# Performance work log

Hardware: AMD Instinct MI355X
Metric: run time of the kernel (lower is better)

The kernel has to match this reference:

```python
import jax, jax.numpy as jnp
import numpy as np

TEMPERATURE = 12.5      # args_temperature
SINKHORN_EPS = 0.05     # entropic regularization replacing exact cv2.EMD
SINKHORN_ITERS = 100


def _sinkhorn_flow(cost, a, b):
    # cost: [N, hw, hw] (rows=query nodes, cols=proto nodes)
    # a: [N, hw] row marginals, b: [N, hw] col marginals (each sums to hw)
    K = jnp.exp(-cost / SINKHORN_EPS)
    v0 = jnp.ones_like(b)

    def body(v, _):
        u = a / (jnp.einsum('nuv,nv->nu', K, v) + 1e-30)
        v = b / (jnp.einsum('nuv,nu->nv', K, u) + 1e-30)
        return v, None

    v, _ = jax.lax.scan(body, v0, None, length=SINKHORN_ITERS)
    u = a / (jnp.einsum('nuv,nv->nu', K, v) + 1e-30)
    return u[:, :, None] * K * v[:, None, :]  # transport plan [N, hw, hw]


def setup_inputs() -> dict:
    key = jax.random.key(0)
    k1, k2 = jax.random.split(key)
    shape = (8, 5, 15, 640, 5, 5)  # (b, n2, n1, c, h, w)
    return {
        'in_support': jax.random.normal(k1, shape, jnp.float32),
        'in_query': jax.random.normal(k2, shape, jnp.float32),
    }


def reference(in_support, in_query):
    b, n2, n1, c, h, w = in_support.shape
    N, hw = b * n2 * n1, h * w
    S = in_support.reshape(N, c, hw)  # support/proto nodes
    Q = in_query.reshape(N, c, hw)    # query nodes

    # get_weight_vector: relu(<node, global-avg-pool(other)>) + 0.001
    w1 = jax.nn.relu(jnp.einsum('nck,nc->nk', Q, S.mean(-1))) + 0.001  # query-side
    w2 = jax.nn.relu(jnp.einsum('nck,nc->nk', S, Q.mean(-1))) + 0.001  # proto-side

    # normalize_feature: subtract per-sample channel mean ('center')
    S = S - S.mean(axis=1, keepdims=True)
    Q = Q - Q.mean(axis=1, keepdims=True)

    # cosine similarity map: sim[u, v] = cos(query_node_u, proto_node_v)
    Sn = S / jnp.maximum(jnp.linalg.norm(S, axis=1, keepdims=True), 1e-8)
    Qn = Q / jnp.maximum(jnp.linalg.norm(Q, axis=1, keepdims=True), 1e-8)
    sim = jnp.einsum('ncu,ncv->nuv', Qn, Sn)  # [N, hw, hw]

    # emd marginals: (w + 1e-5) rescaled so each sums to hw
    a = w1 + 1e-5
    a = a * (hw / a.sum(-1, keepdims=True))
    bm = w2 + 1e-5
    bm = bm * (hw / bm.sum(-1, keepdims=True))

    # OT flow on cost = 1 - sim (flow treated as a constant, like cv2 detach)
    flow = jax.lax.stop_gradient(_sinkhorn_flow(1.0 - sim, a, bm))

    return (sim * flow).sum((-1, -2)) * (TEMPERATURE / hw)  # logits [N]
```

## Files before the change

### kernel.cpp

```cpp
#include <hip/hip_runtime.h>

typedef short bf16x8 __attribute__((ext_vector_type(8)));
typedef float f32x4  __attribute__((ext_vector_type(4)));

constexpr int C  = 640;
constexpr int HW = 25;
constexpr int CHUNK  = 128;
constexpr int NCHUNK = 5;

__device__ __forceinline__ float rl(float x, int lane) {
  return __uint_as_float(__builtin_amdgcn_readlane(__float_as_uint(x), lane));
}

__device__ __forceinline__ void split_bf16(float x, unsigned& h, unsigned& l) {
  unsigned u = __float_as_uint(x);
  unsigned hb = (u + 0x7FFFu + ((u >> 16) & 1u)) >> 16;
  float hf = __uint_as_float(hb << 16);
  float lo = x - hf;
  unsigned ul = __float_as_uint(lo);
  unsigned lb = (ul + 0x7FFFu + ((ul >> 16) & 1u)) >> 16;
  h = hb; l = lb;
}

__global__ __launch_bounds__(256) void emd_fused(
    const float* __restrict__ support, const float* __restrict__ query,
    float* __restrict__ out)
{
  const int n = blockIdx.x, tid = threadIdx.x;

  __shared__ __attribute__((aligned(16))) unsigned short planes[4 * 32 * CHUNK];
  __shared__ float G[625];
  __shared__ float scr[4][200];
  __shared__ float sQv[25], sSv[25], nqv[25], nsv[25], amv[25], bmv[25], scal[2];

  const float* Qg = query   + (size_t)n * (C * HW);
  const float* Sg = support + (size_t)n * (C * HW);

  for (int g = tid; g < 448; g += 256) {
    int pl = g / 112, rem = g % 112;
    int r = 25 + rem / 16, cq = rem % 16;
    *reinterpret_cast<uint4*>(reinterpret_cast<char*>(planes) +
                              ((pl * 32 + r) * CHUNK + cq * 8) * 2) = make_uint4(0, 0, 0, 0);
  }

  const int k = tid % 25;
  f32x4 acc[2][2];
  {
    f32x4 z = {0.f, 0.f, 0.f, 0.f};
    acc[0][0] = z; acc[0][1] = z; acc[1][0] = z; acc[1][1] = z;
  }
  float mQ = 0.f, mQ2 = 0.f, mS = 0.f, mS2 = 0.f;

  for (int ch = 0; ch < NCHUNK; ++ch) {
    if (ch) __syncthreads();
    if (tid < 200) {
      #pragma unroll
      for (int p = 0; p < 4; ++p) {
        const int gm = tid + (p & 1) * 200;
        const int cg = gm / 25;
        const int mat = p >> 1;
        const float* src = (mat ? Sg : Qg) + ((size_t)ch * CHUNK + cg * 8) * HW + k;
        float x[8];
        #pragma unroll
        for (int j = 0; j < 8; ++j) x[j] = src[j * 25];
        if (mat == 0) {
          #pragma unroll
          for (int j = 0; j < 8; ++j) { mQ += x[j]; mQ2 = fmaf(x[j], x[j], mQ2); }
        } else {
          #pragma unroll
          for (int j = 0; j < 8; ++j) { mS += x[j]; mS2 = fmaf(x[j], x[j], mS2); }
        }
        unsigned hwd[4], lwd[4];
        #pragma unroll
        for (int jj = 0; jj < 4; ++jj) {
          unsigned h0, l0, h1, l1;
          split_bf16(x[2 * jj], h0, l0);
          split_bf16(x[2 * jj + 1], h1, l1);
          hwd[jj] = h0 | (h1 << 16);
          lwd[jj] = l0 | (l1 << 16);
        }
        const int xo = (k & 15) << 4;
        char* pb = reinterpret_cast<char*>(planes);
        int bh = ((((mat * 2 + 0) * 32 + k) * CHUNK + cg * 8) * 2) ^ xo;
        int bl = ((((mat * 2 + 1) * 32 + k) * CHUNK + cg * 8) * 2) ^ xo;
        *reinterpret_cast<uint4*>(pb + bh) = make_uint4(hwd[0], hwd[1], hwd[2], hwd[3]);
        *reinterpret_cast<uint4*>(pb + bl) = make_uint4(lwd[0], lwd[1], lwd[2], lwd[3]);
      }
    }
    __syncthreads();
    if (tid < 64) {
      const char* pb = reinterpret_cast<const char*>(planes);
      #pragma unroll
      for (int s = 0; s < 4; ++s) {
        const int cb = (s * 32 + ((tid >> 4) * 8)) * 2;
        bf16x8 Ah[2], Al[2], Bh[2], Bl[2];
        #pragma unroll
        for (int tr = 0; tr < 2; ++tr) {
          const int r = (tid & 15) + 16 * tr;
          const int xo = (r & 15) << 4;
          Ah[tr] = *reinterpret_cast<const bf16x8*>(pb + ((((0 * 32 + r) * CHUNK) * 2 + cb) ^ xo));
          Al[tr] = *reinterpret_cast<const bf16x8*>(pb + ((((1 * 32 + r) * CHUNK) * 2 + cb) ^ xo));
          Bh[tr] = *reinterpret_cast<const bf16x8*>(pb + ((((2 * 32 + r) * CHUNK) * 2 + cb) ^ xo));
          Bl[tr] = *reinterpret_cast<const bf16x8*>(pb + ((((3 * 32 + r) * CHUNK) * 2 + cb) ^ xo));
        }
        #pragma unroll
        for (int tr = 0; tr < 2; ++tr)
          #pragma unroll
          for (int tc = 0; tc < 2; ++tc) {
            acc[tr][tc] = __builtin_amdgcn_mfma_f32_16x16x32_bf16(Ah[tr], Bh[tc], acc[tr][tc], 0, 0, 0);
            acc[tr][tc] = __builtin_amdgcn_mfma_f32_16x16x32_bf16(Ah[tr], Bl[tc], acc[tr][tc], 0, 0, 0);
            acc[tr][tc] = __builtin_amdgcn_mfma_f32_16x16x32_bf16(Al[tr], Bh[tc], acc[tr][tc], 0, 0, 0);
          }
      }
    }
  }

  if (tid < 64) {
    #pragma unroll
    for (int tr = 0; tr < 2; ++tr)
      #pragma unroll
      for (int tc = 0; tc < 2; ++tc)
        #pragma unroll
        for (int i = 0; i < 4; ++i) {
          int u = tr * 16 + (tid >> 4) * 4 + i;
          int v = tc * 16 + (tid & 15);
          if (u < 25 && v < 25) G[u * 25 + v] = acc[tr][tc][i];
        }
  }
  if (tid < 200) { scr[0][tid] = mQ; scr[1][tid] = mQ2; scr[2][tid] = mS; scr[3][tid] = mS2; }
  __syncthreads();

  if (tid < 25) {
    float s = 0.f, ss = 0.f;
    #pragma unroll
    for (int i = 0; i < 8; ++i) { s += scr[0][tid + 25 * i]; ss += scr[1][tid + 25 * i]; }
    sQv[tid] = s;
    float var = ss - s * s * (1.f / C);
    nqv[tid] = fmaxf(sqrtf(fmaxf(var, 0.f)), 1e-8f);
    float rs = 0.f;
    #pragma unroll
    for (int j = 0; j < 25; ++j) rs += G[tid * 25 + j];
    amv[tid] = fmaxf(rs * (1.f / 25.f), 0.f) + 0.001f + 1e-5f;
  } else if (tid >= 32 && tid < 57) {
    int v = tid - 32;
    float s = 0.f, ss = 0.f;
    #pragma unroll
    for (int i = 0; i < 8; ++i) { s += scr[2][v + 25 * i]; ss += scr[3][v + 25 * i]; }
    sSv[v] = s;
    float var = ss - s * s * (1.f / C);
    nsv[v] = fmaxf(sqrtf(fmaxf(var, 0.f)), 1e-8f);
    float cs = 0.f;
    #pragma unroll
    for (int u = 0; u < 25; ++u) cs += G[u * 25 + v];
    bmv[v] = fmaxf(cs * (1.f / 25.f), 0.f) + 0.001f + 1e-5f;
  }
  __syncthreads();
  if (tid == 0)  { float s = 0.f; for (int i = 0; i < 25; ++i) s += amv[i]; scal[0] = 25.f / s; }
  if (tid == 64) { float s = 0.f; for (int i = 0; i < 25; ++i) s += bmv[i]; scal[1] = 25.f / s; }
  __syncthreads();
  for (int p = tid; p < 625; p += 256) {
    int u = p / 25, v = p % 25;
    float cov = G[p] - sQv[u] * sSv[v] * (1.f / C);
    G[p] = cov / (nqv[u] * nsv[v]);
  }
  __syncthreads();

  if (tid >= 64) return;
  const int lane = tid;
  const int u = (lane < 25) ? lane : 24;
  float simr[25], Krow[25], Kcol[25];
  #pragma unroll
  for (int j = 0; j < 25; ++j) simr[j] = G[u * 25 + j];
  #pragma unroll
  for (int j = 0; j < 25; ++j) Kcol[j] = __expf(-20.f * (1.f - G[j * 25 + u]));
  #pragma unroll
  for (int j = 0; j < 25; ++j) Krow[j] = __expf(-20.f * (1.f - simr[j]));
  const float a_u = amv[u] * scal[0], b_u = bmv[u] * scal[1];

  float vv = 1.0f, uu = 0.0f, vold = 1.0f;
  #pragma unroll 1
  for (int it = 0; it < 100; ++it) {
    float s0 = 0, s1 = 0, s2 = 0, s3 = 0, s4 = 0;
    #pragma unroll
    for (int j = 0; j < 25; j += 5) {
      s0 = fmaf(Krow[j + 0], rl(vv, j + 0), s0);
      s1 = fmaf(Krow[j + 1], rl(vv, j + 1), s1);
      s2 = fmaf(Krow[j + 2], rl(vv, j + 2), s2);
      s3 = fmaf(Krow[j + 3], rl(vv, j + 3), s3);
      s4 = fmaf(Krow[j + 4], rl(vv, j + 4), s4);
    }
    uu = a_u * __builtin_amdgcn_rcpf(((((s0 + s1) + (s2 + s3)) + s4) + 1e-30f));

    s0 = s1 = s2 = s3 = s4 = 0;
    #pragma unroll
    for (int j = 0; j < 25; j += 5) {
      s0 = fmaf(Kcol[j + 0], rl(uu, j + 0), s0);
      s1 = fmaf(Kcol[j + 1], rl(uu, j + 1), s1);
      s2 = fmaf(Kcol[j + 2], rl(uu, j + 2), s2);
      s3 = fmaf(Kcol[j + 3], rl(uu, j + 3), s3);
      s4 = fmaf(Kcol[j + 4], rl(uu, j + 4), s4);
    }
    vv = b_u * __builtin_amdgcn_rcpf(((((s0 + s1) + (s2 + s3)) + s4) + 1e-30f));

    if ((it & 7) == 7) {
      bool conv = fabsf(vv - vold) <= 1e-5f * fabsf(vv);
      if (__all(conv)) break;
      vold = vv;
    }
  }
  {
    float s0 = 0, s1 = 0, s2 = 0, s3 = 0, s4 = 0;
    #pragma unroll
    for (int j = 0; j < 25; j += 5) {
      s0 = fmaf(Krow[j + 0], rl(vv, j + 0), s0);
      s1 = fmaf(Krow[j + 1], rl(vv, j + 1), s1);
      s2 = fmaf(Krow[j + 2], rl(vv, j + 2), s2);
      s3 = fmaf(Krow[j + 3], rl(vv, j + 3), s3);
      s4 = fmaf(Krow[j + 4], rl(vv, j + 4), s4);
    }
    uu = a_u * __builtin_amdgcn_rcpf(((((s0 + s1) + (s2 + s3)) + s4) + 1e-30f));
  }

  float pr = 0.f;
  if (lane < 25) {
    float t0 = 0.f;
    #pragma unroll
    for (int j = 0; j < 25; ++j)
      t0 = fmaf(simr[j] * Krow[j], rl(vv, j), t0);
    pr = uu * t0;
  }
  #pragma unroll
  for (int off = 32; off; off >>= 1) pr += __shfl_xor(pr, off);
  if (lane == 0) out[n] = pr * 0.5f;
}

extern "C" void kernel_launch(void* const* d_in, const int* in_sizes, int n_in,
                              void* d_out, int out_size, void* d_ws, size_t ws_size,
                              hipStream_t stream) {
  const float* support = (const float*)d_in[0];
  const float* query   = (const float*)d_in[1];
  float* out = (float*)d_out;
  const int N = in_sizes[0] / (C * HW);
  emd_fused<<<dim3(N), dim3(256), 0, stream>>>(support, query, out);
}
```

Before: 30.79 us.

## Split Gram MFMA across four waves with direct register loads, drop LDS staging

Replaces the single-wave MFMA Gram computation fed by LDS bf16 planes with all four waves each handling a quarter of the channels. Each wave loads its fragments straight from global memory into registers and splits them into hi/lo bf16 by truncation with perm. The per-wave partial accumulators and moments are then reduced through shared memory. It also checks Sinkhorn convergence every 4 iterations instead of 8. This removes LDS round trips and several barriers and lets all waves issue MFMA, but truncation changes the hi/lo split numerics and the global loads are strided and uncoalesced.

```diff
diff --git a/kernel.cpp b/kernel.cpp
--- a/kernel.cpp
+++ b/kernel.cpp
@@ -5,21 +5,17 @@
 
 constexpr int C  = 640;
 constexpr int HW = 25;
-constexpr int CHUNK  = 128;
-constexpr int NCHUNK = 5;
 
 __device__ __forceinline__ float rl(float x, int lane) {
   return __uint_as_float(__builtin_amdgcn_readlane(__float_as_uint(x), lane));
 }
 
-__device__ __forceinline__ void split_bf16(float x, unsigned& h, unsigned& l) {
-  unsigned u = __float_as_uint(x);
-  unsigned hb = (u + 0x7FFFu + ((u >> 16) & 1u)) >> 16;
-  float hf = __uint_as_float(hb << 16);
-  float lo = x - hf;
-  unsigned ul = __float_as_uint(lo);
-  unsigned lb = (ul + 0x7FFFu + ((ul >> 16) & 1u)) >> 16;
-  h = hb; l = lb;
+__device__ __forceinline__ void packpair(float x0, float x1, unsigned& h, unsigned& l) {
+  unsigned u0 = __float_as_uint(x0), u1 = __float_as_uint(x1);
+  h = __builtin_amdgcn_perm(u1, u0, 0x07060302u);
+  float l0 = x0 - __uint_as_float(u0 & 0xFFFF0000u);
+  float l1 = x1 - __uint_as_float(u1 & 0xFFFF0000u);
+  l = __builtin_amdgcn_perm(__float_as_uint(l1), __float_as_uint(l0), 0x07060302u);
 }
 
 __global__ __launch_bounds__(256) void emd_fused(
@@ -27,113 +23,103 @@
     float* __restrict__ out)
 {
   const int n = blockIdx.x, tid = threadIdx.x;
-
-  __shared__ __attribute__((aligned(16))) unsigned short planes[4 * 32 * CHUNK];
+  const int wid = tid >> 6, lane = tid & 63;
+  const int lg = lane >> 4, lr = lane & 15;
+
+  __shared__ float accbuf[4][64][16];
+  __shared__ float mombuf[4][8][64];
   __shared__ float G[625];
-  __shared__ float scr[4][200];
   __shared__ float sQv[25], sSv[25], nqv[25], nsv[25], amv[25], bmv[25], scal[2];
 
-  const float* Qg = query   + (size_t)n * (C * HW);
-  const float* Sg = support + (size_t)n * (C * HW);
-
-  for (int g = tid; g < 448; g += 256) {
-    int pl = g / 112, rem = g % 112;
-    int r = 25 + rem / 16, cq = rem % 16;
-    *reinterpret_cast<uint4*>(reinterpret_cast<char*>(planes) +
-                              ((pl * 32 + r) * CHUNK + cq * 8) * 2) = make_uint4(0, 0, 0, 0);
-  }
-
-  const int k = tid % 25;
+  const float* Qg = query   + (size_t)n * C * HW;
+  const float* Sg = support + (size_t)n * C * HW;
+
   f32x4 acc[2][2];
   {
     f32x4 z = {0.f, 0.f, 0.f, 0.f};
     acc[0][0] = z; acc[0][1] = z; acc[1][0] = z; acc[1][1] = z;
   }
-  float mQ = 0.f, mQ2 = 0.f, mS = 0.f, mS2 = 0.f;
-
-  for (int ch = 0; ch < NCHUNK; ++ch) {
-    if (ch) __syncthreads();
-    if (tid < 200) {
-      #pragma unroll
-      for (int p = 0; p < 4; ++p) {
-        const int gm = tid + (p & 1) * 200;
-        const int cg = gm / 25;
-        const int mat = p >> 1;
-        const float* src = (mat ? Sg : Qg) + ((size_t)ch * CHUNK + cg * 8) * HW + k;
-        float x[8];
-        #pragma unroll
-        for (int j = 0; j < 8; ++j) x[j] = src[j * 25];
-        if (mat == 0) {
-          #pragma unroll
-          for (int j = 0; j < 8; ++j) { mQ += x[j]; mQ2 = fmaf(x[j], x[j], mQ2); }
-        } else {
-          #pragma unroll
-          for (int j = 0; j < 8; ++j) { mS += x[j]; mS2 = fmaf(x[j], x[j], mS2); }
-        }
-        unsigned hwd[4], lwd[4];
-        #pragma unroll
-        for (int jj = 0; jj < 4; ++jj) {
-          unsigned h0, l0, h1, l1;
-          split_bf16(x[2 * jj], h0, l0);
-          split_bf16(x[2 * jj + 1], h1, l1);
-          hwd[jj] = h0 | (h1 << 16);
-          lwd[jj] = l0 | (l1 << 16);
-        }
-        const int xo = (k & 15) << 4;
-        char* pb = reinterpret_cast<char*>(planes);
-        int bh = ((((mat * 2 + 0) * 32 + k) * CHUNK + cg * 8) * 2) ^ xo;
-        int bl = ((((mat * 2 + 1) * 32 + k) * CHUNK + cg * 8) * 2) ^ xo;
-        *reinterpret_cast<uint4*>(pb + bh) = make_uint4(hwd[0], hwd[1], hwd[2], hwd[3]);
-        *reinterpret_cast<uint4*>(pb + bl) = make_uint4(lwd[0], lwd[1], lwd[2], lwd[3]);
-      }
-    }
-    __syncthreads();
-    if (tid < 64) {
-      const char* pb = reinterpret_cast<const char*>(planes);
-      #pragma unroll
-      for (int s = 0; s < 4; ++s) {
-        const int cb = (s * 32 + ((tid >> 4) * 8)) * 2;
-        bf16x8 Ah[2], Al[2], Bh[2], Bl[2];
-        #pragma unroll
-        for (int tr = 0; tr < 2; ++tr) {
-          const int r = (tid & 15) + 16 * tr;
-          const int xo = (r & 15) << 4;
-          Ah[tr] = *reinterpret_cast<const bf16x8*>(pb + ((((0 * 32 + r) * CHUNK) * 2 + cb) ^ xo));
-          Al[tr] = *reinterpret_cast<const bf16x8*>(pb + ((((1 * 32 + r) * CHUNK) * 2 + cb) ^ xo));
-          Bh[tr] = *reinterpret_cast<const bf16x8*>(pb + ((((2 * 32 + r) * CHUNK) * 2 + cb) ^ xo));
-          Bl[tr] = *reinterpret_cast<const bf16x8*>(pb + ((((3 * 32 + r) * CHUNK) * 2 + cb) ^ xo));
-        }
-        #pragma unroll
-        for (int tr = 0; tr < 2; ++tr)
-          #pragma unroll
-          for (int tc = 0; tc < 2; ++tc) {
-            acc[tr][tc] = __builtin_amdgcn_mfma_f32_16x16x32_bf16(Ah[tr], Bh[tc], acc[tr][tc], 0, 0, 0);
-            acc[tr][tc] = __builtin_amdgcn_mfma_f32_16x16x32_bf16(Ah[tr], Bl[tc], acc[tr][tc], 0, 0, 0);
-            acc[tr][tc] = __builtin_amdgcn_mfma_f32_16x16x32_bf16(Al[tr], Bh[tc], acc[tr][tc], 0, 0, 0);
-          }
-      }
-    }
-  }
+  float mq[2] = {0.f, 0.f}, mq2[2] = {0.f, 0.f};
+  float ms[2] = {0.f, 0.f}, ms2[2] = {0.f, 0.f};
+
+  #pragma unroll 1
+  for (int s = 0; s < 5; ++s) {
+    const int c0 = wid * 160 + s * 32 + lg * 8;
+    const float* qb = Qg + c0 * HW;
+    const float* sb = Sg + c0 * HW;
+    bf16x8 Ah[2], Al[2], Bh[2], Bl[2];
+    #pragma unroll
+    for (int t = 0; t < 2; ++t) {
+      const int row = t * 16 + lr;
+      const bool ok = row < 25;
+      float xq[8], xs[8];
+      #pragma unroll
+      for (int j = 0; j < 8; ++j) {
+        xq[j] = ok ? qb[j * HW + row] : 0.f;
+        xs[j] = ok ? sb[j * HW + row] : 0.f;
+      }
+      #pragma unroll
+      for (int j = 0; j < 8; ++j) {
+        mq[t] += xq[j]; mq2[t] = fmaf(xq[j], xq[j], mq2[t]);
+        ms[t] += xs[j]; ms2[t] = fmaf(xs[j], xs[j], ms2[t]);
+      }
+      union { unsigned u[4]; bf16x8 v; } ah, al, bh, bl;
+      #pragma unroll
+      for (int jj = 0; jj < 4; ++jj) {
+        packpair(xq[2 * jj], xq[2 * jj + 1], ah.u[jj], al.u[jj]);
+        packpair(xs[2 * jj], xs[2 * jj + 1], bh.u[jj], bl.u[jj]);
+      }
+      Ah[t] = ah.v; Al[t] = al.v; Bh[t] = bh.v; Bl[t] = bl.v;
+    }
+    #pragma unroll
+    for (int tr = 0; tr < 2; ++tr)
+      #pragma unroll
+      for (int tc = 0; tc < 2; ++tc) {
+        acc[tr][tc] = __builtin_amdgcn_mfma_f32_16x16x32_bf16(Ah[tr], Bh[tc], acc[tr][tc], 0, 0, 0);
+        acc[tr][tc] = __builtin_amdgcn_mfma_f32_16x16x32_bf16(Ah[tr], Bl[tc], acc[tr][tc], 0, 0, 0);
+        acc[tr][tc] = __builtin_amdgcn_mfma_f32_16x16x32_bf16(Al[tr], Bh[tc], acc[tr][tc], 0, 0, 0);
+      }
+  }
+
+  #pragma unroll
+  for (int tr = 0; tr < 2; ++tr)
+    #pragma unroll
+    for (int tc = 0; tc < 2; ++tc)
+      *reinterpret_cast<f32x4*>(&accbuf[wid][lane][(tr * 2 + tc) * 4]) = acc[tr][tc];
+  mombuf[wid][0][lane] = mq[0];  mombuf[wid][1][lane] = mq[1];
+  mombuf[wid][2][lane] = mq2[0]; mombuf[wid][3][lane] = mq2[1];
+  mombuf[wid][4][lane] = ms[0];  mombuf[wid][5][lane] = ms[1];
+  mombuf[wid][6][lane] = ms2[0]; mombuf[wid][7][lane] = ms2[1];
+  __syncthreads();
 
   if (tid < 64) {
     #pragma unroll
-    for (int tr = 0; tr < 2; ++tr)
-      #pragma unroll
-      for (int tc = 0; tc < 2; ++tc)
-        #pragma unroll
-        for (int i = 0; i < 4; ++i) {
-          int u = tr * 16 + (tid >> 4) * 4 + i;
-          int v = tc * 16 + (tid & 15);
-          if (u < 25 && v < 25) G[u * 25 + v] = acc[tr][tc][i];
-        }
-  }
-  if (tid < 200) { scr[0][tid] = mQ; scr[1][tid] = mQ2; scr[2][tid] = mS; scr[3][tid] = mS2; }
+    for (int q = 0; q < 4; ++q) {
+      f32x4 rsum = *reinterpret_cast<const f32x4*>(&accbuf[0][lane][q * 4]);
+      #pragma unroll
+      for (int w = 1; w < 4; ++w)
+        rsum += *reinterpret_cast<const f32x4*>(&accbuf[w][lane][q * 4]);
+      const int tr = q >> 1, tc = q & 1;
+      #pragma unroll
+      for (int i = 0; i < 4; ++i) {
+        int u = tr * 16 + (lane >> 4) * 4 + i;
+        int v = tc * 16 + (lane & 15);
+        if (u < 25 && v < 25) G[u * 25 + v] = rsum[i];
+      }
+    }
+  }
   __syncthreads();
 
   if (tid < 25) {
+    const int t = (tid < 16) ? 0 : 1, rr = tid - t * 16;
     float s = 0.f, ss = 0.f;
     #pragma unroll
-    for (int i = 0; i < 8; ++i) { s += scr[0][tid + 25 * i]; ss += scr[1][tid + 25 * i]; }
+    for (int w = 0; w < 4; ++w)
+      #pragma unroll
+      for (int gg = 0; gg < 4; ++gg) {
+        s  += mombuf[w][0 + t][gg * 16 + rr];
+        ss += mombuf[w][2 + t][gg * 16 + rr];
+      }
     sQv[tid] = s;
     float var = ss - s * s * (1.f / C);
     nqv[tid] = fmaxf(sqrtf(fmaxf(var, 0.f)), 1e-8f);
@@ -142,10 +128,16 @@
     for (int j = 0; j < 25; ++j) rs += G[tid * 25 + j];
     amv[tid] = fmaxf(rs * (1.f / 25.f), 0.f) + 0.001f + 1e-5f;
   } else if (tid >= 32 && tid < 57) {
-    int v = tid - 32;
+    const int v = tid - 32;
+    const int t = (v < 16) ? 0 : 1, rr = v - t * 16;
     float s = 0.f, ss = 0.f;
     #pragma unroll
-    for (int i = 0; i < 8; ++i) { s += scr[2][v + 25 * i]; ss += scr[3][v + 25 * i]; }
+    for (int w = 0; w < 4; ++w)
+      #pragma unroll
+      for (int gg = 0; gg < 4; ++gg) {
+        s  += mombuf[w][4 + t][gg * 16 + rr];
+        ss += mombuf[w][6 + t][gg * 16 + rr];
+      }
     sSv[v] = s;
     float var = ss - s * s * (1.f / C);
     nsv[v] = fmaxf(sqrtf(fmaxf(var, 0.f)), 1e-8f);
@@ -166,8 +158,7 @@
   __syncthreads();
 
   if (tid >= 64) return;
-  const int lane = tid;
-  const int u = (lane < 25) ? lane : 24;
+  const int u = (tid < 25) ? tid : 24;
   float simr[25], Krow[25], Kcol[25];
   #pragma unroll
   for (int j = 0; j < 25; ++j) simr[j] = G[u * 25 + j];
@@ -202,7 +193,7 @@
     }
     vv = b_u * __builtin_amdgcn_rcpf(((((s0 + s1) + (s2 + s3)) + s4) + 1e-30f));
 
-    if ((it & 7) == 7) {
+    if ((it & 3) == 3) {
       bool conv = fabsf(vv - vold) <= 1e-5f * fabsf(vv);
       if (__all(conv)) break;
       vold = vv;
@@ -222,7 +213,7 @@
   }
 
   float pr = 0.f;
-  if (lane < 25) {
+  if (tid < 25) {
     float t0 = 0.f;
     #pragma unroll
     for (int j = 0; j < 25; ++j)
@@ -231,7 +222,7 @@
   }
   #pragma unroll
   for (int off = 32; off; off >>= 1) pr += __shfl_xor(pr, off);
-  if (lane == 0) out[n] = pr * 0.5f;
+  if (tid == 0) out[n] = pr * 0.5f;
 }
 
 extern "C" void kernel_launch(void* const* d_in, const int* in_sizes, int n_in,
```

Result: faster. 25.80 us (-16.2%).
